# Optimization experiments

Measured on AMD Instinct MI355X. Metric: run time of the kernel, lower is better.

The kernel has to match this reference:

```python
import jax, jax.numpy as jnp
import numpy as np

R, C, H, W = 500, 512, 38, 38      # rois, VGG channels, feature-map HxW (img 608 / 16)
K, HID, POOL, SCALE = 20, 4096, 3, 16
FEAT = C * POOL * POOL             # 4608, matches fc6 in_features


def setup_inputs():
    key = jax.random.key(0)
    ks = jax.random.split(key, 12)
    fmap = jax.random.normal(ks[0], (C, H, W), dtype=jnp.float32)
    # ROIs in original image coords (x1,y1,x2,y2); width/height >= 48 px so that
    # after /16 + floor every ROI is non-degenerate (none filtered out).
    x1 = jax.random.randint(ks[1], (R,), 0, 288)
    y1 = jax.random.randint(ks[2], (R,), 0, 288)
    bw = jax.random.randint(ks[3], (R,), 48, 304)
    bh = jax.random.randint(ks[4], (R,), 48, 304)
    rois = jnp.stack([x1, y1, x1 + bw, y1 + bh], axis=1).astype(jnp.float32)
    label = jax.random.bernoulli(ks[5], 0.3, (K,)).astype(jnp.float32)
    s = 0.01
    W6 = jax.random.normal(ks[6], (FEAT, HID), jnp.float32) * s
    b6 = jnp.zeros((HID,), jnp.float32)
    W7 = jax.random.normal(ks[7], (HID, HID), jnp.float32) * s
    b7 = jnp.zeros((HID,), jnp.float32)
    W8c = jax.random.normal(ks[8], (HID, K), jnp.float32) * s
    b8c = jnp.zeros((K,), jnp.float32)
    W8d = jax.random.normal(ks[9], (HID, K), jnp.float32) * s
    b8d = jnp.zeros((K,), jnp.float32)
    return dict(fmap=fmap, rois=rois, label=label, W6=W6, b6=b6, W7=W7, b7=b7,
                W8c=W8c, b8c=b8c, W8d=W8d, b8d=b8d)


def _roi_pool(fmap, rois):
    # scaled_rois = origin_rois / 16, sliced as integer indices (floor)
    sc = jnp.floor(rois / SCALE).astype(jnp.int32)          # [R,4]
    x1, y1, x2, y2 = sc[:, 0], sc[:, 1], sc[:, 2], sc[:, 3]

    def binmask(lo, hi, size):
        # adaptive-max-pool bins: [lo + floor(j*L/3), lo + ceil((j+1)*L/3))
        L = hi - lo                                          # [R]
        j = jnp.arange(POOL)
        start = lo[:, None] + (j[None, :] * L[:, None]) // POOL
        end = lo[:, None] + (-((-(j[None, :] + 1) * L[:, None]) // POOL))
        pos = jnp.arange(size)
        return (pos[None, None, :] >= start[:, :, None]) & (pos[None, None, :] < end[:, :, None])

    cm = binmask(x1, x2, W)                                  # [R,3,W]
    rm = binmask(y1, y2, H)                                  # [R,3,H]
    neg = jnp.finfo(fmap.dtype).min
    # max over x within each x-bin: [R,C,H,3]
    tmp = jnp.max(jnp.where(cm[:, None, None, :, :], fmap[None, :, :, None, :], neg), axis=-1)
    # max over y within each y-bin: [R,C,3,3]
    pooled = jnp.max(jnp.where(rm[:, None, :, :, None], tmp[:, :, None, :, :], neg), axis=3)
    return pooled.reshape(R, FEAT), sc.astype(jnp.float32)


def _spatial_reg(scores, fc7, rois_sc, label):
    # faithful to original: argsort ascending, index 0 taken as the reference box,
    # and bboxes_iou interprets (x1,y1,x2,y2) as (x,y,w,h) — replicated as-is.
    idx = jnp.argsort(scores, axis=0)                        # [R,K]

    def per_class(idx_k, s_k, lab_k):
        h, rest = idx_k[0], idx_k[1:]
        hb = rois_sc[h]                                      # [4]
        rb = rois_sc[rest]                                   # [R-1,4]
        b1x2, b1y2 = rb[:, 0] + rb[:, 2], rb[:, 1] + rb[:, 3]
        b2x2, b2y2 = hb[0] + hb[2], hb[1] + hb[3]
        iw = jnp.clip(jnp.minimum(b1x2, b2x2) - jnp.maximum(rb[:, 0], hb[0]) + 1, 0)
        ih = jnp.clip(jnp.minimum(b1y2, b2y2) - jnp.maximum(rb[:, 1], hb[1]) + 1, 0)
        inter = iw * ih
        a1 = (b1x2 - rb[:, 0] + 1) * (b1y2 - rb[:, 1] + 1)
        a2 = (b2x2 - hb[0] + 1) * (b2y2 - hb[1] + 1)
        iou = inter / (a1 + a2 - inter)
        m = (iou > 0.6).astype(fc7.dtype)                    # [R-1]
        rf = fc7[rest] * m[:, None]
        diff = (rf - fc7[h]) * s_k[rest][:, None]
        return lab_k * 0.5 * jnp.sum(diff * diff)

    regs = jax.vmap(per_class)(idx.T, scores.T, label)       # [K]
    return jnp.sum(regs) / K


def reference(fmap, rois, label, W6, b6, W7, b7, W8c, b8c, W8d, b8d):
    feat, rois_sc = _roi_pool(fmap, rois)                    # [R,4608]
    fc6 = feat @ W6 + b6
    fc7 = fc6 @ W7 + b7
    pc = jax.nn.softmax(fc7 @ W8c + b8c, axis=1)             # per-roi over classes
    pd = jax.nn.softmax(fc7 @ W8d + b8d, axis=0)             # per-class over rois
    scores = pc * pd                                         # [R,K]
    out = jnp.sum(scores, axis=0)                            # [K], in (0,1)
    bce = -jnp.mean(label * jnp.log(out) + (1.0 - label) * jnp.log(1.0 - out))
    reg = _spatial_reg(scores, fc7, rois_sc, label)
    return scores, bce + reg, reg
```

## Files before the change

kernel.cpp:

```cpp
#include <hip/hip_runtime.h>
#include <cstdint>
#include <cstddef>

#define DEV __device__ __forceinline__

typedef __bf16 bf16_t;
typedef __bf16 bf16x8 __attribute__((ext_vector_type(8)));
typedef float  f32x4  __attribute__((ext_vector_type(4)));
typedef float  f32x2  __attribute__((ext_vector_type(2)));
typedef unsigned int u32x4 __attribute__((ext_vector_type(4)));

DEV bf16_t f2bf(float x) { return (bf16_t)x; }

constexpr int R_ = 500, C_ = 512, H_ = 38, W_ = 38, K_ = 20;
constexpr int HID = 4096, FEAT = 4608, MP = 512;
constexpr int HW = H_ * W_;

constexpr size_t alup(size_t x) { return (x + 255) & ~(size_t)255; }
constexpr size_t O_FMT  = 0;
constexpr size_t O_RSC  = alup(O_FMT  + (size_t)HW*C_*4);
constexpr size_t O_FEAT = alup(O_RSC  + (size_t)R_*4*4);
constexpr size_t O_FC6  = alup(O_FEAT + (size_t)MP*FEAT*2);
constexpr size_t O_FC7  = alup(O_FC6  + (size_t)MP*HID*2);
constexpr size_t O_PC   = alup(O_FC7  + (size_t)MP*HID*4);
constexpr size_t O_LD   = alup(O_PC   + (size_t)R_*K_*4);
constexpr size_t O_AN   = alup(O_LD   + (size_t)R_*K_*4);
constexpr size_t O_OS   = alup(O_AN   + (size_t)MP*4);
constexpr size_t O_HI   = alup(O_OS   + (size_t)K_*4);
constexpr size_t O_D    = alup(O_HI   + (size_t)K_*4);
constexpr size_t O_W8T  = alup(O_D    + (size_t)R_*K_*4);
constexpr size_t O_PART = alup(O_W8T  + (size_t)2*K_*HID*4);
constexpr size_t O_HP   = O_PART;
constexpr size_t O_DP   = O_PART + (size_t)4*1024*1024;

__global__ void __launch_bounds__(256) k_transpose(const float* __restrict__ fmap,
                                                   float* __restrict__ fmapt) {
    __shared__ float tile[32][33];
    int p0 = blockIdx.x * 32, c0 = blockIdx.y * 32;
    int tx = threadIdx.x & 31, ty = threadIdx.x >> 5;
#pragma unroll
    for (int i = 0; i < 4; ++i) {
        int c = c0 + ty + i*8, p = p0 + tx;
        tile[ty + i*8][tx] = (p < HW) ? fmap[(size_t)c*HW + p] : 0.f;
    }
    __syncthreads();
#pragma unroll
    for (int i = 0; i < 4; ++i) {
        int p = p0 + ty + i*8, c = c0 + tx;
        if (p < HW) fmapt[(size_t)p*C_ + c] = tile[tx][ty + i*8];
    }
}

__global__ void __launch_bounds__(256) k_w8t(const float* __restrict__ W8c,
                                             const float* __restrict__ W8d,
                                             float* __restrict__ W8T) {
    int k = blockIdx.x;
    const float* src = (k < K_) ? W8c : W8d;
    int kk = (k < K_) ? k : k - K_;
    for (int i = threadIdx.x; i < HID; i += 256)
        W8T[(size_t)k*HID + i] = src[(size_t)i*K_ + kk];
}

__global__ void __launch_bounds__(256) k_roipool(const float* __restrict__ fmapt,
                                                 const float* __restrict__ rois,
                                                 bf16_t* __restrict__ feat,
                                                 float* __restrict__ rois_sc) {
    int r = blockIdx.x, bin = blockIdx.y, t = threadIdx.x;
    if (r >= R_) {
        feat[(size_t)r*FEAT + (size_t)t*9       + bin] = (bf16_t)0.f;
        feat[(size_t)r*FEAT + (size_t)(t+256)*9 + bin] = (bf16_t)0.f;
        return;
    }
    int x1 = (int)floorf(rois[r*4+0] * 0.0625f);
    int y1 = (int)floorf(rois[r*4+1] * 0.0625f);
    int x2 = (int)floorf(rois[r*4+2] * 0.0625f);
    int y2 = (int)floorf(rois[r*4+3] * 0.0625f);
    if (bin == 0 && t == 0) {
        rois_sc[r*4+0] = (float)x1; rois_sc[r*4+1] = (float)y1;
        rois_sc[r*4+2] = (float)x2; rois_sc[r*4+3] = (float)y2;
    }
    int Lx = x2 - x1, Ly = y2 - y1;
    int pr = bin / 3, px = bin - pr*3;
    int rs = y1 + (pr*Ly)/3, re = y1 + ((pr+1)*Ly + 2)/3;
    int cs = x1 + (px*Lx)/3, ce = x1 + ((px+1)*Lx + 2)/3;
    float m0 = -3.402823466e38f, m1 = -3.402823466e38f;
    for (int y = rs; y < re; ++y) {
        const float* rowp = fmapt + (size_t)(y*W_)*C_;
        for (int x = cs; x < ce; ++x) {
            const float* p = rowp + (size_t)x*C_;
            m0 = fmaxf(m0, p[t]);
            m1 = fmaxf(m1, p[t + 256]);
        }
    }
    feat[(size_t)r*FEAT + (size_t)t*9       + bin] = f2bf(m0);
    feat[(size_t)r*FEAT + (size_t)(t+256)*9 + bin] = f2bf(m1);
}

__global__ void __launch_bounds__(256, 3)
k_gemm(const bf16_t* __restrict__ A, const float* __restrict__ B,
       float* __restrict__ part, int KDIM, int nts) {
    __shared__ bf16_t Asm[2][128*64];
    __shared__ bf16_t Bsm[2][64*64];
    const int t = threadIdx.x;
    const int lane = t & 63, wid = t >> 6;
    const int wr = wid >> 1, wc = wid & 1;

    const int flat = blockIdx.x + 64*blockIdx.y + 256*blockIdx.z;
    const int v = (flat & 7) * 128 + (flat >> 3);
    const int by = v & 3, bx = (v >> 2) & 63, bz = v >> 8;

    const int brow = by * 128, bcol = bx * 64;
    const int kt0 = bz * nts;

    f32x4 acc[4][2] = {};
    f32x2 br[8];
    const int n2 = t & 31, kgl = t >> 5;

    auto stage_A = [&](int kt, int buf) {
        const bf16_t* Ag = A + (size_t)brow*KDIM + kt*64;
#pragma unroll
        for (int i = 0; i < 4; ++i) {
            int s = t + i*256;
            int row = s >> 3;
            int kb = (s & 7) ^ ((row >> 1) & 7);
            const bf16_t* src = Ag + (size_t)row*KDIM + kb*8;
            bf16_t* dst = &Asm[buf][(size_t)(i*256 + (t & ~63)) * 8];
            __builtin_amdgcn_global_load_lds(
                (const __attribute__((address_space(1))) void*)src,
                (__attribute__((address_space(3))) void*)dst, 16, 0, 0);
        }
    };
    auto load_B = [&](int kt) {
        const float* src = B + (size_t)(kt*64 + kgl*8)*HID + bcol + 2*n2;
#pragma unroll
        for (int j = 0; j < 8; ++j)
            br[j] = *reinterpret_cast<const f32x2*>(src + (size_t)j*HID);
    };
    auto write_B = [&](int buf) {
        const int sw = n2 & 7;
        bf16x8 v0, v1;
#pragma unroll
        for (int j = 0; j < 8; ++j) { v0[j] = f2bf(br[j].x); v1[j] = f2bf(br[j].y); }
        *reinterpret_cast<u32x4*>(&Bsm[buf][(size_t)((2*n2    )*8 + (kgl ^ sw)) * 8]) = *reinterpret_cast<u32x4*>(&v0);
        *reinterpret_cast<u32x4*>(&Bsm[buf][(size_t)((2*n2 + 1)*8 + (kgl ^ sw)) * 8]) = *reinterpret_cast<u32x4*>(&v1);
    };

    stage_A(kt0, 0);
    load_B(kt0);
    write_B(0);
    __syncthreads();

    for (int it = 0; it < nts; ++it) {
        const int cur = it & 1;
        if (it + 1 < nts) { stage_A(kt0 + it + 1, cur ^ 1); load_B(kt0 + it + 1); }
#pragma unroll
        for (int kk = 0; kk < 2; ++kk) {
            const int kb = kk*4 + (lane >> 4);
            bf16x8 af[4], bfr[2];
#pragma unroll
            for (int m = 0; m < 4; ++m) {
                int row = wr*64 + m*16 + (lane & 15);
                af[m] = *reinterpret_cast<const bf16x8*>(
                    &Asm[cur][(size_t)(row*8 + (kb ^ ((row >> 1) & 7))) * 8]);
            }
#pragma unroll
            for (int n = 0; n < 2; ++n) {
                int nn = wc*32 + n*16 + (lane & 15);
                bfr[n] = *reinterpret_cast<const bf16x8*>(
                    &Bsm[cur][(size_t)(nn*8 + (kb ^ ((nn >> 1) & 7))) * 8]);
            }
#pragma unroll
            for (int m = 0; m < 4; ++m)
#pragma unroll
                for (int n = 0; n < 2; ++n)
                    acc[m][n] = __builtin_amdgcn_mfma_f32_16x16x32_bf16(af[m], bfr[n], acc[m][n], 0, 0, 0);
        }
        if (it + 1 < nts) { write_B(cur ^ 1); __syncthreads(); }
    }

    float* dst = part + (size_t)bz * MP * HID;
#pragma unroll
    for (int m = 0; m < 4; ++m) {
        int row0 = brow + wr*64 + m*16 + ((lane >> 4) << 2);
#pragma unroll
        for (int n = 0; n < 2; ++n) {
            int col = bcol + wc*32 + n*16 + (lane & 15);
#pragma unroll
            for (int j = 0; j < 4; ++j)
                dst[(size_t)(row0 + j)*HID + col] = acc[m][n][j];
        }
    }
}

__global__ void __launch_bounds__(256) k_reduce(const float* __restrict__ part,
                                                const float* __restrict__ bias,
                                                bf16_t* __restrict__ ob, float* __restrict__ of,
                                                int ksplit) {
    size_t idx = ((size_t)blockIdx.x*256 + threadIdx.x) * 4;
    f32x4 s = *reinterpret_cast<const f32x4*>(part + idx);
    for (int ss = 1; ss < ksplit; ++ss)
        s += *reinterpret_cast<const f32x4*>(part + (size_t)ss*MP*HID + idx);
    int col = (int)(idx & (HID - 1));
    s += *reinterpret_cast<const f32x4*>(bias + col);
    if (ob) {
#pragma unroll
        for (int j = 0; j < 4; ++j) ob[idx + j] = f2bf(s[j]);
    } else {
        *reinterpret_cast<f32x4*>(of + idx) = s;
    }
}

template<int NOUT, bool SELF>
__global__ void __launch_bounds__(256) k_dotcols(const float* __restrict__ fc7,
        const float* __restrict__ Bmat, const int* __restrict__ bidx,
        float* __restrict__ partial) {
    constexpr int NO = NOUT + (SELF ? 1 : 0);
    constexpr int SLICE = NOUT*16 + 4;
    __shared__ float Bs[8 * SLICE];
    const int rb = blockIdx.x, kb = blockIdx.y, t = threadIdx.x;
    const int k0 = kb * 128;
    for (int i = t; i < NOUT*32; i += 256) {
        int o = i >> 5, c = i & 31;
        const float* src = bidx ? fc7 + (size_t)bidx[o]*HID : Bmat + (size_t)o*HID;
        f32x4 v = *reinterpret_cast<const f32x4*>(src + k0 + c*4);
        *reinterpret_cast<f32x4*>(&Bs[(c >> 2)*SLICE + o*16 + (c & 3)*4]) = v;
    }
    __syncthreads();
    const int lane = t & 63, w = t >> 6;
    const int ri = lane >> 3, kk = lane & 7;
    const int r0 = rb*64 + w*16 + ri*2;
    f32x4 x0[4], x1[4];
    const float* f0 = fc7 + (size_t)r0*HID + k0 + kk*16;
#pragma unroll
    for (int j = 0; j < 4; ++j) {
        x0[j] = *reinterpret_cast<const f32x4*>(f0 + j*4);
        x1[j] = *reinterpret_cast<const f32x4*>(f0 + HID + j*4);
    }
    float acc0[NO], acc1[NO];
#pragma unroll
    for (int o = 0; o < NOUT; ++o) {
        f32x4 s0 = {}, s1 = {};
#pragma unroll
        for (int j = 0; j < 4; ++j) {
            f32x4 wv = *reinterpret_cast<const f32x4*>(&Bs[kk*SLICE + o*16 + j*4]);
            s0 += x0[j] * wv;
            s1 += x1[j] * wv;
        }
        acc0[o] = s0[0]+s0[1]+s0[2]+s0[3];
        acc1[o] = s1[0]+s1[1]+s1[2]+s1[3];
    }
    if (SELF) {
        f32x4 s0 = {}, s1 = {};
#pragma unroll
        for (int j = 0; j < 4; ++j) { s0 += x0[j]*x0[j]; s1 += x1[j]*x1[j]; }
        acc0[NO-1] = s0[0]+s0[1]+s0[2]+s0[3];
        acc1[NO-1] = s1[0]+s1[1]+s1[2]+s1[3];
    }
#pragma unroll
    for (int o = 0; o < NO; ++o) {
#pragma unroll
        for (int m = 1; m < 8; m <<= 1) {
            acc0[o] += __shfl_xor(acc0[o], m, 64);
            acc1[o] += __shfl_xor(acc1[o], m, 64);
        }
    }
    if (kk == 0) {
#pragma unroll
        for (int o = 0; o < NO; ++o) {
            partial[((size_t)kb*MP + r0    )*NO + o] = acc0[o];
            partial[((size_t)kb*MP + r0 + 1)*NO + o] = acc1[o];
        }
    }
}

__global__ void __launch_bounds__(64) k_headred(const float* __restrict__ hpart,
        const float* __restrict__ b8c, const float* __restrict__ b8d,
        float* __restrict__ pc, float* __restrict__ ld, float* __restrict__ An) {
    int r = blockIdx.x, t = threadIdx.x;
    __shared__ float lcs[20];
    if (t < 41) {
        float s = 0.f;
        for (int kb = 0; kb < 32; ++kb) s += hpart[((size_t)kb*MP + r)*41 + t];
        if (t < 20)      lcs[t] = s + b8c[t];
        else if (t < 40) ld[r*K_ + (t-20)] = s + b8d[t-20];
        else             An[r] = s;
    }
    __syncthreads();
    if (t == 0) {
        float mx = lcs[0];
#pragma unroll
        for (int k = 1; k < 20; ++k) mx = fmaxf(mx, lcs[k]);
        float sum = 0.f, e[20];
#pragma unroll
        for (int k = 0; k < 20; ++k) { e[k] = expf(lcs[k] - mx); sum += e[k]; }
        float inv = 1.f / sum;
#pragma unroll
        for (int k = 0; k < 20; ++k) pc[r*K_ + k] = e[k] * inv;
    }
}

__global__ void __launch_bounds__(64) k_dmatred(const float* __restrict__ dpart,
                                                float* __restrict__ D) {
    int r = blockIdx.x, t = threadIdx.x;
    if (t < 20) {
        float s = 0.f;
        for (int kb = 0; kb < 32; ++kb) s += dpart[((size_t)kb*MP + r)*20 + t];
        D[r*K_ + t] = s;
    }
}

__global__ void __launch_bounds__(256) k_pd(const float* __restrict__ ld,
        const float* __restrict__ pc, float* __restrict__ scores,
        float* __restrict__ out_sum, int* __restrict__ h_idx) {
    int k = blockIdx.x, t = threadIdx.x;
    __shared__ float sh[4];
    float m = -3.402823466e38f;
    for (int r = t; r < R_; r += 256) m = fmaxf(m, ld[r*K_ + k]);
    for (int off = 1; off < 64; off <<= 1) m = fmaxf(m, __shfl_xor(m, off, 64));
    if ((t & 63) == 0) sh[t >> 6] = m;
    __syncthreads();
    m = fmaxf(fmaxf(sh[0], sh[1]), fmaxf(sh[2], sh[3]));
    __syncthreads();
    float s = 0.f;
    for (int r = t; r < R_; r += 256) s += expf(ld[r*K_ + k] - m);
    for (int off = 1; off < 64; off <<= 1) s += __shfl_xor(s, off, 64);
    if ((t & 63) == 0) sh[t >> 6] = s;
    __syncthreads();
    s = sh[0] + sh[1] + sh[2] + sh[3];
    float inv = 1.f / s;

    float osum = 0.f, bv = 3.402823466e38f; int bi = 0x7fffffff;
    for (int r = t; r < R_; r += 256) {
        float p  = expf(ld[r*K_ + k] - m) * inv;
        float sc = pc[r*K_ + k] * p;
        scores[r*K_ + k] = sc;
        osum += sc;
        if (sc < bv || (sc == bv && r < bi)) { bv = sc; bi = r; }
    }
    for (int off = 1; off < 64; off <<= 1) osum += __shfl_xor(osum, off, 64);
    for (int off = 1; off < 64; off <<= 1) {
        float v2 = __shfl_xor(bv, off, 64);
        int   i2 = __shfl_xor(bi, off, 64);
        if (v2 < bv || (v2 == bv && i2 < bi)) { bv = v2; bi = i2; }
    }
    __shared__ float so[4], mv[4]; __shared__ int mi[4];
    if ((t & 63) == 0) { so[t >> 6] = osum; mv[t >> 6] = bv; mi[t >> 6] = bi; }
    __syncthreads();
    if (t == 0) {
        out_sum[k] = so[0] + so[1] + so[2] + so[3];
        float v = mv[0]; int i = mi[0];
        for (int w = 1; w < 4; ++w)
            if (mv[w] < v || (mv[w] == v && mi[w] < i)) { v = mv[w]; i = mi[w]; }
        h_idx[k] = i;
    }
}

__global__ void __launch_bounds__(256) k_final(const float* __restrict__ out_sum,
        const int* __restrict__ h_idx, const float* __restrict__ label,
        const float* __restrict__ scores, const float* __restrict__ D,
        const float* __restrict__ An, const float* __restrict__ rois_sc,
        float* __restrict__ dout) {
    int t = threadIdx.x;
    __shared__ float bsh[20];
    if (t < 20) {
        float o = out_sum[t], lab = label[t];
        bsh[t] = lab * logf(o) + (1.f - lab) * logf(1.f - o);
    }
    __syncthreads();

    float rp = 0.f;
    for (int i = t; i < R_*K_; i += 256) {
        int r = i / 20, k = i - r*20;
        int h = h_idx[k];
        if (r == h) continue;
        float lab = label[k];
        if (lab == 0.f) continue;
        float s = scores[r*K_ + k];
        const float* rb = rois_sc + r*4;
        const float* hb = rois_sc + h*4;
        float b1x2 = rb[0] + rb[2], b1y2 = rb[1] + rb[3];
        float b2x2 = hb[0] + hb[2], b2y2 = hb[1] + hb[3];
        float iw = fmaxf(fminf(b1x2, b2x2) - fmaxf(rb[0], hb[0]) + 1.f, 0.f);
        float ih = fmaxf(fminf(b1y2, b2y2) - fmaxf(rb[1], hb[1]) + 1.f, 0.f);
        float inter = iw * ih;
        float a1 = (b1x2 - rb[0] + 1.f) * (b1y2 - rb[1] + 1.f);
        float a2 = (b2x2 - hb[0] + 1.f) * (b2y2 - hb[1] + 1.f);
        float iou = inter / (a1 + a2 - inter);
        float mm = (iou > 0.6f) ? 1.f : 0.f;
        float term = mm * (An[r] - 2.f * D[r*K_ + k]) + An[h];
        rp += lab * 0.5f * s * s * term;
    }
    for (int off = 1; off < 64; off <<= 1) rp += __shfl_xor(rp, off, 64);
    __shared__ float rsh[4];
    if ((t & 63) == 0) rsh[t >> 6] = rp;
    __syncthreads();
    if (t == 0) {
        float reg = (rsh[0] + rsh[1] + rsh[2] + rsh[3]) / (float)K_;
        float b = 0.f;
        for (int k = 0; k < 20; ++k) b += bsh[k];
        float bce = -b / (float)K_;
        dout[R_*K_]     = bce + reg;
        dout[R_*K_ + 1] = reg;
    }
}

extern "C" void kernel_launch(void* const* d_in, const int* in_sizes, int n_in,
                              void* d_out, int out_size, void* d_ws, size_t ws_size,
                              hipStream_t stream) {
    const float* fmap  = (const float*)d_in[0];
    const float* rois  = (const float*)d_in[1];
    const float* label = (const float*)d_in[2];
    const float* W6    = (const float*)d_in[3];
    const float* b6    = (const float*)d_in[4];
    const float* W7    = (const float*)d_in[5];
    const float* b7    = (const float*)d_in[6];
    const float* W8c   = (const float*)d_in[7];
    const float* b8c   = (const float*)d_in[8];
    const float* W8d   = (const float*)d_in[9];
    const float* b8d   = (const float*)d_in[10];
    char* ws = (char*)d_ws;
    float* out = (float*)d_out;

    float*  fmapt = (float*)(ws + O_FMT);
    float*  roisc = (float*)(ws + O_RSC);
    bf16_t* feat  = (bf16_t*)(ws + O_FEAT);
    bf16_t* fc6   = (bf16_t*)(ws + O_FC6);
    float*  fc7   = (float*)(ws + O_FC7);
    float*  pc    = (float*)(ws + O_PC);
    float*  ld    = (float*)(ws + O_LD);
    float*  An    = (float*)(ws + O_AN);
    float*  osum  = (float*)(ws + O_OS);
    int*    hidx  = (int*)(ws + O_HI);
    float*  Dm    = (float*)(ws + O_D);
    float*  w8t   = (float*)(ws + O_W8T);
    float*  part  = (float*)(ws + O_PART);
    float*  hpart = (float*)(ws + O_HP);
    float*  dpart = (float*)(ws + O_DP);

    const int ksplit = 4;

    k_transpose<<<dim3((HW + 31)/32, C_/32), dim3(256), 0, stream>>>(fmap, fmapt);
    k_w8t      <<<dim3(2*K_),   dim3(256), 0, stream>>>(W8c, W8d, w8t);
    k_roipool  <<<dim3(MP, 9),  dim3(256), 0, stream>>>(fmapt, rois, feat, roisc);

    k_gemm  <<<dim3(HID/64, MP/128, ksplit), dim3(256), 0, stream>>>(feat, W6, part, FEAT, (FEAT/64)/ksplit);
    k_reduce<<<dim3((MP*HID)/1024), dim3(256), 0, stream>>>(part, b6, fc6, (float*)nullptr, ksplit);

    k_gemm  <<<dim3(HID/64, MP/128, ksplit), dim3(256), 0, stream>>>(fc6, W7, part, HID, (HID/64)/ksplit);
    k_reduce<<<dim3((MP*HID)/1024), dim3(256), 0, stream>>>(part, b7, (bf16_t*)nullptr, fc7, ksplit);

    k_dotcols<40, true><<<dim3(MP/64, HID/128), dim3(256), 0, stream>>>(fc7, w8t, (const int*)nullptr, hpart);
    k_headred<<<dim3(R_), dim3(64), 0, stream>>>(hpart, b8c, b8d, pc, ld, An);
    k_pd     <<<dim3(K_), dim3(256), 0, stream>>>(ld, pc, out, osum, hidx);
    k_dotcols<20, false><<<dim3(MP/64, HID/128), dim3(256), 0, stream>>>(fc7, (const float*)nullptr, hidx, dpart);
    k_dmatred<<<dim3(R_), dim3(64), 0, stream>>>(dpart, Dm);
    k_final  <<<dim3(1),  dim3(256), 0, stream>>>(osum, hidx, label, out, Dm, An, roisc, out);
}
```

Before: 199.1 us.

## Widen GEMM tile to 128x128 and deepen A/B prefetch pipeline

The fc6/fc7 GEMM moves from 128x64 to 128x128 output tiles, so each wave computes a 4x4 set of MFMA accumulators and each B load is reused across more rows. The A tile now uses triple-buffered async global-to-LDS loads and B uses two register sets, so loads run two k-steps ahead. Barriers become explicit s_waitcnt plus s_barrier calls. This halves the grid to 512 blocks and raises register and LDS use, which lowers the occupancy target from 3 to 2 blocks per CU. The main loop assumes an even tile count per split.

```diff
diff --git a/kernel.cpp b/kernel.cpp
--- a/kernel.cpp
+++ b/kernel.cpp
@@ -96,27 +96,27 @@
     feat[(size_t)r*FEAT + (size_t)(t+256)*9 + bin] = f2bf(m1);
 }
 
-__global__ void __launch_bounds__(256, 3)
+__global__ void __launch_bounds__(256, 2)
 k_gemm(const bf16_t* __restrict__ A, const float* __restrict__ B,
        float* __restrict__ part, int KDIM, int nts) {
-    __shared__ bf16_t Asm[2][128*64];
-    __shared__ bf16_t Bsm[2][64*64];
+    __shared__ bf16_t Asm[3][128*64];
+    __shared__ bf16_t Bsm[2][128*64];
     const int t = threadIdx.x;
     const int lane = t & 63, wid = t >> 6;
     const int wr = wid >> 1, wc = wid & 1;
 
-    const int flat = blockIdx.x + 64*blockIdx.y + 256*blockIdx.z;
-    const int v = (flat & 7) * 128 + (flat >> 3);
-    const int by = v & 3, bx = (v >> 2) & 63, bz = v >> 8;
-
-    const int brow = by * 128, bcol = bx * 64;
+    const int flat = blockIdx.x + 32*blockIdx.y + 128*blockIdx.z;
+    const int q = 16 * gridDim.z;
+    const int v = (flat & 7) * q + (flat >> 3);
+    const int by = v & 3, bx = (v >> 2) & 31, bz = v >> 7;
+
+    const int brow = by * 128, bcol = bx * 128;
     const int kt0 = bz * nts;
 
-    f32x4 acc[4][2] = {};
-    f32x2 br[8];
-    const int n2 = t & 31, kgl = t >> 5;
-
-    auto stage_A = [&](int kt, int buf) {
+    f32x4 acc[4][4] = {};
+    const int n2 = t & 63, kgl = t >> 6;
+
+    auto stage_A = [&](int kt, bf16_t* dstbuf) {
         const bf16_t* Ag = A + (size_t)brow*KDIM + kt*64;
 #pragma unroll
         for (int i = 0; i < 4; ++i) {
@@ -124,58 +124,81 @@
             int row = s >> 3;
             int kb = (s & 7) ^ ((row >> 1) & 7);
             const bf16_t* src = Ag + (size_t)row*KDIM + kb*8;
-            bf16_t* dst = &Asm[buf][(size_t)(i*256 + (t & ~63)) * 8];
+            bf16_t* dst = dstbuf + (size_t)(i*256 + (t & ~63)) * 8;
             __builtin_amdgcn_global_load_lds(
                 (const __attribute__((address_space(1))) void*)src,
                 (__attribute__((address_space(3))) void*)dst, 16, 0, 0);
         }
     };
-    auto load_B = [&](int kt) {
-        const float* src = B + (size_t)(kt*64 + kgl*8)*HID + bcol + 2*n2;
-#pragma unroll
-        for (int j = 0; j < 8; ++j)
+    auto load_B = [&](int kt, f32x2* br) {
+        const float* src = B + (size_t)(kt*64 + kgl*16)*HID + bcol + 2*n2;
+#pragma unroll
+        for (int j = 0; j < 16; ++j)
             br[j] = *reinterpret_cast<const f32x2*>(src + (size_t)j*HID);
     };
-    auto write_B = [&](int buf) {
+    auto write_B = [&](f32x2* br, bf16_t* buf) {
         const int sw = n2 & 7;
         bf16x8 v0, v1;
 #pragma unroll
-        for (int j = 0; j < 8; ++j) { v0[j] = f2bf(br[j].x); v1[j] = f2bf(br[j].y); }
-        *reinterpret_cast<u32x4*>(&Bsm[buf][(size_t)((2*n2    )*8 + (kgl ^ sw)) * 8]) = *reinterpret_cast<u32x4*>(&v0);
-        *reinterpret_cast<u32x4*>(&Bsm[buf][(size_t)((2*n2 + 1)*8 + (kgl ^ sw)) * 8]) = *reinterpret_cast<u32x4*>(&v1);
+        for (int j = 0; j < 8; ++j) { v0[j] = f2bf(br[j].x); v1[j] = f2bf(br[j+8].x); }
+        *reinterpret_cast<u32x4*>(&buf[(size_t)((2*n2)*8 + ((kgl*2    ) ^ sw)) * 8]) = *reinterpret_cast<u32x4*>(&v0);
+        *reinterpret_cast<u32x4*>(&buf[(size_t)((2*n2)*8 + ((kgl*2 + 1) ^ sw)) * 8]) = *reinterpret_cast<u32x4*>(&v1);
+#pragma unroll
+        for (int j = 0; j < 8; ++j) { v0[j] = f2bf(br[j].y); v1[j] = f2bf(br[j+8].y); }
+        *reinterpret_cast<u32x4*>(&buf[(size_t)((2*n2+1)*8 + ((kgl*2    ) ^ sw)) * 8]) = *reinterpret_cast<u32x4*>(&v0);
+        *reinterpret_cast<u32x4*>(&buf[(size_t)((2*n2+1)*8 + ((kgl*2 + 1) ^ sw)) * 8]) = *reinterpret_cast<u32x4*>(&v1);
     };
 
-    stage_A(kt0, 0);
-    load_B(kt0);
-    write_B(0);
-    __syncthreads();
-
-    for (int it = 0; it < nts; ++it) {
-        const int cur = it & 1;
-        if (it + 1 < nts) { stage_A(kt0 + it + 1, cur ^ 1); load_B(kt0 + it + 1); }
+    bf16_t* pa0 = &Asm[0][0]; bf16_t* pa1 = &Asm[1][0]; bf16_t* pa2 = &Asm[2][0];
+    bf16_t* pb0 = &Bsm[0][0]; bf16_t* pb1 = &Bsm[1][0];
+    f32x2 brA[16], brB[16];
+
+    stage_A(kt0 + 0, pa0);
+    load_B (kt0 + 0, brA);
+    stage_A(kt0 + 1, pa1);
+    load_B (kt0 + 1, brB);
+    write_B(brA, pb0);
+    asm volatile("s_waitcnt lgkmcnt(0)" ::: "memory");
+    __builtin_amdgcn_s_barrier();
+    __builtin_amdgcn_sched_barrier(0);
+
+    auto body = [&](int tt, f32x2* prev, f32x2* next) {
+        if (tt + 2 < nts) { stage_A(kt0 + tt + 2, pa2); load_B(kt0 + tt + 2, next); }
 #pragma unroll
         for (int kk = 0; kk < 2; ++kk) {
             const int kb = kk*4 + (lane >> 4);
-            bf16x8 af[4], bfr[2];
+            bf16x8 af[4], bfr[4];
 #pragma unroll
             for (int m = 0; m < 4; ++m) {
                 int row = wr*64 + m*16 + (lane & 15);
                 af[m] = *reinterpret_cast<const bf16x8*>(
-                    &Asm[cur][(size_t)(row*8 + (kb ^ ((row >> 1) & 7))) * 8]);
+                    pa0 + (size_t)(row*8 + (kb ^ ((row >> 1) & 7))) * 8);
             }
 #pragma unroll
-            for (int n = 0; n < 2; ++n) {
-                int nn = wc*32 + n*16 + (lane & 15);
+            for (int n = 0; n < 4; ++n) {
+                int nn = wc*64 + n*16 + (lane & 15);
                 bfr[n] = *reinterpret_cast<const bf16x8*>(
-                    &Bsm[cur][(size_t)(nn*8 + (kb ^ ((nn >> 1) & 7))) * 8]);
+                    pb0 + (size_t)(nn*8 + (kb ^ ((nn >> 1) & 7))) * 8);
             }
 #pragma unroll
             for (int m = 0; m < 4; ++m)
 #pragma unroll
-                for (int n = 0; n < 2; ++n)
+                for (int n = 0; n < 4; ++n)
                     acc[m][n] = __builtin_amdgcn_mfma_f32_16x16x32_bf16(af[m], bfr[n], acc[m][n], 0, 0, 0);
         }
-        if (it + 1 < nts) { write_B(cur ^ 1); __syncthreads(); }
+        if (tt + 1 < nts) {
+            write_B(prev, pb1);
+            asm volatile("s_waitcnt lgkmcnt(0)" ::: "memory");
+            __builtin_amdgcn_s_barrier();
+            __builtin_amdgcn_sched_barrier(0);
+        }
+        bf16_t* ta = pa0; pa0 = pa1; pa1 = pa2; pa2 = ta;
+        bf16_t* tb = pb0; pb0 = pb1; pb1 = tb;
+    };
+
+    for (int it = 0; it < nts; it += 2) {
+        body(it,     brB, brA);
+        body(it + 1, brA, brB);
     }
 
     float* dst = part + (size_t)bz * MP * HID;
@@ -183,8 +206,8 @@
     for (int m = 0; m < 4; ++m) {
         int row0 = brow + wr*64 + m*16 + ((lane >> 4) << 2);
 #pragma unroll
-        for (int n = 0; n < 2; ++n) {
-            int col = bcol + wc*32 + n*16 + (lane & 15);
+        for (int n = 0; n < 4; ++n) {
+            int col = bcol + wc*64 + n*16 + (lane & 15);
 #pragma unroll
             for (int j = 0; j < 4; ++j)
                 dst[(size_t)(row0 + j)*HID + col] = acc[m][n][j];
@@ -443,10 +466,10 @@
     k_w8t      <<<dim3(2*K_),   dim3(256), 0, stream>>>(W8c, W8d, w8t);
     k_roipool  <<<dim3(MP, 9),  dim3(256), 0, stream>>>(fmapt, rois, feat, roisc);
 
-    k_gemm  <<<dim3(HID/64, MP/128, ksplit), dim3(256), 0, stream>>>(feat, W6, part, FEAT, (FEAT/64)/ksplit);
+    k_gemm  <<<dim3(HID/128, MP/128, ksplit), dim3(256), 0, stream>>>(feat, W6, part, FEAT, (FEAT/64)/ksplit);
     k_reduce<<<dim3((MP*HID)/1024), dim3(256), 0, stream>>>(part, b6, fc6, (float*)nullptr, ksplit);
 
-    k_gemm  <<<dim3(HID/64, MP/128, ksplit), dim3(256), 0, stream>>>(fc6, W7, part, HID, (HID/64)/ksplit);
+    k_gemm  <<<dim3(HID/128, MP/128, ksplit), dim3(256), 0, stream>>>(fc6, W7, part, HID, (HID/64)/ksplit);
     k_reduce<<<dim3((MP*HID)/1024), dim3(256), 0, stream>>>(part, b7, (bf16_t*)nullptr, fc7, ksplit);
 
     k_dotcols<40, true><<<dim3(MP/64, HID/128), dim3(256), 0, stream>>>(fc7, w8t, (const int*)nullptr, hpart);
```

Measured after the change: 177.9 us, median of 2. 10.6% less time.

## Replace split-K partial buffers with atomic accumulation and enlarge GEMM tiles

Applied to the files above, without the earlier changes.

The split-K GEMM now adds its partial results and a scaled bias straight into zeroed fp32 outputs with atomics. This removes the partial-buffer write and the separate reduce kernels, and the dotcols partial reductions get the same treatment. The GEMM tile widens to 128x128 with split-K raised to 8, and the transpose and W8 prep kernels merge into one launch. This costs memsets, atomic contention, a separate bf16 cast kernel, lower occupancy, and a summation order that is no longer deterministic.

```diff
diff --git a/kernel.cpp b/kernel.cpp
--- a/kernel.cpp
+++ b/kernel.cpp
@@ -15,50 +15,53 @@
 constexpr int R_ = 500, C_ = 512, H_ = 38, W_ = 38, K_ = 20;
 constexpr int HID = 4096, FEAT = 4608, MP = 512;
 constexpr int HW = H_ * W_;
+constexpr int KSPLIT = 8;
 
 constexpr size_t alup(size_t x) { return (x + 255) & ~(size_t)255; }
 constexpr size_t O_FMT  = 0;
 constexpr size_t O_RSC  = alup(O_FMT  + (size_t)HW*C_*4);
 constexpr size_t O_FEAT = alup(O_RSC  + (size_t)R_*4*4);
 constexpr size_t O_FC6  = alup(O_FEAT + (size_t)MP*FEAT*2);
-constexpr size_t O_FC7  = alup(O_FC6  + (size_t)MP*HID*2);
+constexpr size_t O_FC6F = alup(O_FC6  + (size_t)MP*HID*2);
+constexpr size_t O_FC7  = alup(O_FC6F + (size_t)MP*HID*4);
 constexpr size_t O_PC   = alup(O_FC7  + (size_t)MP*HID*4);
 constexpr size_t O_LD   = alup(O_PC   + (size_t)R_*K_*4);
 constexpr size_t O_AN   = alup(O_LD   + (size_t)R_*K_*4);
 constexpr size_t O_OS   = alup(O_AN   + (size_t)MP*4);
 constexpr size_t O_HI   = alup(O_OS   + (size_t)K_*4);
-constexpr size_t O_D    = alup(O_HI   + (size_t)K_*4);
-constexpr size_t O_W8T  = alup(O_D    + (size_t)R_*K_*4);
-constexpr size_t O_PART = alup(O_W8T  + (size_t)2*K_*HID*4);
-constexpr size_t O_HP   = O_PART;
-constexpr size_t O_DP   = O_PART + (size_t)4*1024*1024;
-
-__global__ void __launch_bounds__(256) k_transpose(const float* __restrict__ fmap,
-                                                   float* __restrict__ fmapt) {
-    __shared__ float tile[32][33];
-    int p0 = blockIdx.x * 32, c0 = blockIdx.y * 32;
-    int tx = threadIdx.x & 31, ty = threadIdx.x >> 5;
-#pragma unroll
-    for (int i = 0; i < 4; ++i) {
-        int c = c0 + ty + i*8, p = p0 + tx;
-        tile[ty + i*8][tx] = (p < HW) ? fmap[(size_t)c*HW + p] : 0.f;
-    }
-    __syncthreads();
-#pragma unroll
-    for (int i = 0; i < 4; ++i) {
-        int p = p0 + ty + i*8, c = c0 + tx;
-        if (p < HW) fmapt[(size_t)p*C_ + c] = tile[tx][ty + i*8];
-    }
-}
-
-__global__ void __launch_bounds__(256) k_w8t(const float* __restrict__ W8c,
-                                             const float* __restrict__ W8d,
-                                             float* __restrict__ W8T) {
-    int k = blockIdx.x;
-    const float* src = (k < K_) ? W8c : W8d;
-    int kk = (k < K_) ? k : k - K_;
-    for (int i = threadIdx.x; i < HID; i += 256)
-        W8T[(size_t)k*HID + i] = src[(size_t)i*K_ + kk];
+constexpr size_t O_W8T  = alup(O_HI   + (size_t)K_*4);
+constexpr size_t O_HL   = alup(O_W8T  + (size_t)2*K_*HID*4);
+constexpr size_t O_D    = alup(O_HL   + (size_t)MP*41*4);
+constexpr size_t O_END  = alup(O_D    + (size_t)MP*K_*4);
+
+__global__ void __launch_bounds__(256) k_prep(const float* __restrict__ fmap,
+                                              float* __restrict__ fmapt,
+                                              const float* __restrict__ W8c,
+                                              const float* __restrict__ W8d,
+                                              float* __restrict__ W8T) {
+    int b = blockIdx.x;
+    if (b < 736) {
+        __shared__ float tile[32][33];
+        int p0 = (b % 46) * 32, c0 = (b / 46) * 32;
+        int tx = threadIdx.x & 31, ty = threadIdx.x >> 5;
+#pragma unroll
+        for (int i = 0; i < 4; ++i) {
+            int c = c0 + ty + i*8, p = p0 + tx;
+            tile[ty + i*8][tx] = (p < HW) ? fmap[(size_t)c*HW + p] : 0.f;
+        }
+        __syncthreads();
+#pragma unroll
+        for (int i = 0; i < 4; ++i) {
+            int p = p0 + ty + i*8, c = c0 + tx;
+            if (p < HW) fmapt[(size_t)p*C_ + c] = tile[tx][ty + i*8];
+        }
+    } else {
+        int k = b - 736;
+        const float* src = (k < K_) ? W8c : W8d;
+        int kk = (k < K_) ? k : k - K_;
+        for (int i = threadIdx.x; i < HID; i += 256)
+            W8T[(size_t)k*HID + i] = src[(size_t)i*K_ + kk];
+    }
 }
 
 __global__ void __launch_bounds__(256) k_roipool(const float* __restrict__ fmapt,
@@ -96,25 +99,26 @@
     feat[(size_t)r*FEAT + (size_t)(t+256)*9 + bin] = f2bf(m1);
 }
 
-__global__ void __launch_bounds__(256, 3)
+__global__ void __launch_bounds__(256, 2)
 k_gemm(const bf16_t* __restrict__ A, const float* __restrict__ B,
-       float* __restrict__ part, int KDIM, int nts) {
+       float* __restrict__ outF32, const float* __restrict__ bias, float bscale,
+       int KDIM, int nts) {
     __shared__ bf16_t Asm[2][128*64];
-    __shared__ bf16_t Bsm[2][64*64];
+    __shared__ bf16_t Bsm[2][128*64];
     const int t = threadIdx.x;
     const int lane = t & 63, wid = t >> 6;
     const int wr = wid >> 1, wc = wid & 1;
 
-    const int flat = blockIdx.x + 64*blockIdx.y + 256*blockIdx.z;
+    const int flat = blockIdx.x + 32*blockIdx.y + 128*blockIdx.z;
     const int v = (flat & 7) * 128 + (flat >> 3);
-    const int by = v & 3, bx = (v >> 2) & 63, bz = v >> 8;
-
-    const int brow = by * 128, bcol = bx * 64;
+    const int by = v & 3, bz = (v >> 2) & 7, bx = v >> 5;
+
+    const int brow = by * 128, bcol = bx * 128;
     const int kt0 = bz * nts;
 
-    f32x4 acc[4][2] = {};
-    f32x2 br[8];
-    const int n2 = t & 31, kgl = t >> 5;
+    f32x4 acc[4][4] = {};
+    f32x2 br[16];
+    const int n2 = t & 63, kgl = t >> 6;
 
     auto stage_A = [&](int kt, int buf) {
         const bf16_t* Ag = A + (size_t)brow*KDIM + kt*64;
@@ -131,18 +135,22 @@
         }
     };
     auto load_B = [&](int kt) {
-        const float* src = B + (size_t)(kt*64 + kgl*8)*HID + bcol + 2*n2;
-#pragma unroll
-        for (int j = 0; j < 8; ++j)
+        const float* src = B + (size_t)(kt*64 + kgl*16)*HID + bcol + 2*n2;
+#pragma unroll
+        for (int j = 0; j < 16; ++j)
             br[j] = *reinterpret_cast<const f32x2*>(src + (size_t)j*HID);
     };
     auto write_B = [&](int buf) {
         const int sw = n2 & 7;
         bf16x8 v0, v1;
 #pragma unroll
-        for (int j = 0; j < 8; ++j) { v0[j] = f2bf(br[j].x); v1[j] = f2bf(br[j].y); }
-        *reinterpret_cast<u32x4*>(&Bsm[buf][(size_t)((2*n2    )*8 + (kgl ^ sw)) * 8]) = *reinterpret_cast<u32x4*>(&v0);
-        *reinterpret_cast<u32x4*>(&Bsm[buf][(size_t)((2*n2 + 1)*8 + (kgl ^ sw)) * 8]) = *reinterpret_cast<u32x4*>(&v1);
+        for (int j = 0; j < 8; ++j) { v0[j] = f2bf(br[j].x); v1[j] = f2bf(br[j+8].x); }
+        *reinterpret_cast<u32x4*>(&Bsm[buf][(size_t)((2*n2)*8 + ((kgl*2    ) ^ sw)) * 8]) = *reinterpret_cast<u32x4*>(&v0);
+        *reinterpret_cast<u32x4*>(&Bsm[buf][(size_t)((2*n2)*8 + ((kgl*2 + 1) ^ sw)) * 8]) = *reinterpret_cast<u32x4*>(&v1);
+#pragma unroll
+        for (int j = 0; j < 8; ++j) { v0[j] = f2bf(br[j].y); v1[j] = f2bf(br[j+8].y); }
+        *reinterpret_cast<u32x4*>(&Bsm[buf][(size_t)((2*n2+1)*8 + ((kgl*2    ) ^ sw)) * 8]) = *reinterpret_cast<u32x4*>(&v0);
+        *reinterpret_cast<u32x4*>(&Bsm[buf][(size_t)((2*n2+1)*8 + ((kgl*2 + 1) ^ sw)) * 8]) = *reinterpret_cast<u32x4*>(&v1);
     };
 
     stage_A(kt0, 0);
@@ -156,7 +164,7 @@
 #pragma unroll
         for (int kk = 0; kk < 2; ++kk) {
             const int kb = kk*4 + (lane >> 4);
-            bf16x8 af[4], bfr[2];
+            bf16x8 af[4], bfr[4];
 #pragma unroll
             for (int m = 0; m < 4; ++m) {
                 int row = wr*64 + m*16 + (lane & 15);
@@ -164,56 +172,49 @@
                     &Asm[cur][(size_t)(row*8 + (kb ^ ((row >> 1) & 7))) * 8]);
             }
 #pragma unroll
-            for (int n = 0; n < 2; ++n) {
-                int nn = wc*32 + n*16 + (lane & 15);
+            for (int n = 0; n < 4; ++n) {
+                int nn = wc*64 + n*16 + (lane & 15);
                 bfr[n] = *reinterpret_cast<const bf16x8*>(
                     &Bsm[cur][(size_t)(nn*8 + (kb ^ ((nn >> 1) & 7))) * 8]);
             }
 #pragma unroll
             for (int m = 0; m < 4; ++m)
 #pragma unroll
-                for (int n = 0; n < 2; ++n)
+                for (int n = 0; n < 4; ++n)
                     acc[m][n] = __builtin_amdgcn_mfma_f32_16x16x32_bf16(af[m], bfr[n], acc[m][n], 0, 0, 0);
         }
         if (it + 1 < nts) { write_B(cur ^ 1); __syncthreads(); }
     }
 
-    float* dst = part + (size_t)bz * MP * HID;
 #pragma unroll
     for (int m = 0; m < 4; ++m) {
         int row0 = brow + wr*64 + m*16 + ((lane >> 4) << 2);
 #pragma unroll
-        for (int n = 0; n < 2; ++n) {
-            int col = bcol + wc*32 + n*16 + (lane & 15);
+        for (int n = 0; n < 4; ++n) {
+            int col = bcol + wc*64 + n*16 + (lane & 15);
+            float bv = bias[col] * bscale;
 #pragma unroll
             for (int j = 0; j < 4; ++j)
-                dst[(size_t)(row0 + j)*HID + col] = acc[m][n][j];
-        }
-    }
-}
-
-__global__ void __launch_bounds__(256) k_reduce(const float* __restrict__ part,
-                                                const float* __restrict__ bias,
-                                                bf16_t* __restrict__ ob, float* __restrict__ of,
-                                                int ksplit) {
-    size_t idx = ((size_t)blockIdx.x*256 + threadIdx.x) * 4;
-    f32x4 s = *reinterpret_cast<const f32x4*>(part + idx);
-    for (int ss = 1; ss < ksplit; ++ss)
-        s += *reinterpret_cast<const f32x4*>(part + (size_t)ss*MP*HID + idx);
-    int col = (int)(idx & (HID - 1));
-    s += *reinterpret_cast<const f32x4*>(bias + col);
-    if (ob) {
-#pragma unroll
-        for (int j = 0; j < 4; ++j) ob[idx + j] = f2bf(s[j]);
-    } else {
-        *reinterpret_cast<f32x4*>(of + idx) = s;
-    }
+                unsafeAtomicAdd(&outF32[(size_t)(row0 + j)*HID + col], acc[m][n][j] + bv);
+        }
+    }
+}
+
+__global__ void __launch_bounds__(256) k_cast(const float* __restrict__ in,
+                                              bf16_t* __restrict__ out) {
+    size_t idx = ((size_t)blockIdx.x*256 + threadIdx.x) * 8;
+    f32x4 a = *reinterpret_cast<const f32x4*>(in + idx);
+    f32x4 b = *reinterpret_cast<const f32x4*>(in + idx + 4);
+    bf16x8 v;
+#pragma unroll
+    for (int j = 0; j < 4; ++j) { v[j] = f2bf(a[j]); v[4+j] = f2bf(b[j]); }
+    *reinterpret_cast<bf16x8*>(out + idx) = v;
 }
 
 template<int NOUT, bool SELF>
 __global__ void __launch_bounds__(256) k_dotcols(const float* __restrict__ fc7,
         const float* __restrict__ Bmat, const int* __restrict__ bidx,
-        float* __restrict__ partial) {
+        float* __restrict__ outacc) {
     constexpr int NO = NOUT + (SELF ? 1 : 0);
     constexpr int SLICE = NOUT*16 + 4;
     __shared__ float Bs[8 * SLICE];
@@ -267,20 +268,19 @@
     if (kk == 0) {
 #pragma unroll
         for (int o = 0; o < NO; ++o) {
-            partial[((size_t)kb*MP + r0    )*NO + o] = acc0[o];
-            partial[((size_t)kb*MP + r0 + 1)*NO + o] = acc1[o];
-        }
-    }
-}
-
-__global__ void __launch_bounds__(64) k_headred(const float* __restrict__ hpart,
+            unsafeAtomicAdd(&outacc[(size_t)r0*NO + o],       acc0[o]);
+            unsafeAtomicAdd(&outacc[(size_t)(r0 + 1)*NO + o], acc1[o]);
+        }
+    }
+}
+
+__global__ void __launch_bounds__(64) k_headred(const float* __restrict__ hl,
         const float* __restrict__ b8c, const float* __restrict__ b8d,
         float* __restrict__ pc, float* __restrict__ ld, float* __restrict__ An) {
     int r = blockIdx.x, t = threadIdx.x;
     __shared__ float lcs[20];
     if (t < 41) {
-        float s = 0.f;
-        for (int kb = 0; kb < 32; ++kb) s += hpart[((size_t)kb*MP + r)*41 + t];
+        float s = hl[(size_t)r*41 + t];
         if (t < 20)      lcs[t] = s + b8c[t];
         else if (t < 40) ld[r*K_ + (t-20)] = s + b8d[t-20];
         else             An[r] = s;
@@ -296,16 +296,6 @@
         float inv = 1.f / sum;
 #pragma unroll
         for (int k = 0; k < 20; ++k) pc[r*K_ + k] = e[k] * inv;
-    }
-}
-
-__global__ void __launch_bounds__(64) k_dmatred(const float* __restrict__ dpart,
-                                                float* __restrict__ D) {
-    int r = blockIdx.x, t = threadIdx.x;
-    if (t < 20) {
-        float s = 0.f;
-        for (int kb = 0; kb < 32; ++kb) s += dpart[((size_t)kb*MP + r)*20 + t];
-        D[r*K_ + t] = s;
     }
 }
 
@@ -425,34 +415,33 @@
     float*  roisc = (float*)(ws + O_RSC);
     bf16_t* feat  = (bf16_t*)(ws + O_FEAT);
     bf16_t* fc6   = (bf16_t*)(ws + O_FC6);
+    float*  fc6f  = (float*)(ws + O_FC6F);
     float*  fc7   = (float*)(ws + O_FC7);
     float*  pc    = (float*)(ws + O_PC);
     float*  ld    = (float*)(ws + O_LD);
     float*  An    = (float*)(ws + O_AN);
     float*  osum  = (float*)(ws + O_OS);
     int*    hidx  = (int*)(ws + O_HI);
+    float*  w8t   = (float*)(ws + O_W8T);
+    float*  hl    = (float*)(ws + O_HL);
     float*  Dm    = (float*)(ws + O_D);
-    float*  w8t   = (float*)(ws + O_W8T);
-    float*  part  = (float*)(ws + O_PART);
-    float*  hpart = (float*)(ws + O_HP);
-    float*  dpart = (float*)(ws + O_DP);
-
-    const int ksplit = 4;
-
-    k_transpose<<<dim3((HW + 31)/32, C_/32), dim3(256), 0, stream>>>(fmap, fmapt);
-    k_w8t      <<<dim3(2*K_),   dim3(256), 0, stream>>>(W8c, W8d, w8t);
-    k_roipool  <<<dim3(MP, 9),  dim3(256), 0, stream>>>(fmapt, rois, feat, roisc);
-
-    k_gemm  <<<dim3(HID/64, MP/128, ksplit), dim3(256), 0, stream>>>(feat, W6, part, FEAT, (FEAT/64)/ksplit);
-    k_reduce<<<dim3((MP*HID)/1024), dim3(256), 0, stream>>>(part, b6, fc6, (float*)nullptr, ksplit);
-
-    k_gemm  <<<dim3(HID/64, MP/128, ksplit), dim3(256), 0, stream>>>(fc6, W7, part, HID, (HID/64)/ksplit);
-    k_reduce<<<dim3((MP*HID)/1024), dim3(256), 0, stream>>>(part, b7, (bf16_t*)nullptr, fc7, ksplit);
-
-    k_dotcols<40, true><<<dim3(MP/64, HID/128), dim3(256), 0, stream>>>(fc7, w8t, (const int*)nullptr, hpart);
-    k_headred<<<dim3(R_), dim3(64), 0, stream>>>(hpart, b8c, b8d, pc, ld, An);
+
+    hipMemsetAsync(fc6f, 0, (size_t)MP*HID*4, stream);
+    hipMemsetAsync(fc7,  0, (size_t)MP*HID*4, stream);
+    hipMemsetAsync(hl,   0, O_END - O_HL, stream);
+
+    k_prep   <<<dim3(736 + 2*K_), dim3(256), 0, stream>>>(fmap, fmapt, W8c, W8d, w8t);
+    k_roipool<<<dim3(MP, 9),      dim3(256), 0, stream>>>(fmapt, rois, feat, roisc);
+
+    k_gemm<<<dim3(HID/128, MP/128, KSPLIT), dim3(256), 0, stream>>>(
+        feat, W6, fc6f, b6, 1.f/KSPLIT, FEAT, (FEAT/64)/KSPLIT);
+    k_cast<<<dim3((MP*HID)/2048), dim3(256), 0, stream>>>(fc6f, fc6);
+    k_gemm<<<dim3(HID/128, MP/128, KSPLIT), dim3(256), 0, stream>>>(
+        fc6, W7, fc7, b7, 1.f/KSPLIT, HID, (HID/64)/KSPLIT);
+
+    k_dotcols<40, true><<<dim3(MP/64, HID/128), dim3(256), 0, stream>>>(fc7, w8t, (const int*)nullptr, hl);
+    k_headred<<<dim3(R_), dim3(64), 0, stream>>>(hl, b8c, b8d, pc, ld, An);
     k_pd     <<<dim3(K_), dim3(256), 0, stream>>>(ld, pc, out, osum, hidx);
-    k_dotcols<20, false><<<dim3(MP/64, HID/128), dim3(256), 0, stream>>>(fc7, (const float*)nullptr, hidx, dpart);
-    k_dmatred<<<dim3(R_), dim3(64), 0, stream>>>(dpart, Dm);
+    k_dotcols<20, false><<<dim3(MP/64, HID/128), dim3(256), 0, stream>>>(fc7, (const float*)nullptr, hidx, Dm);
     k_final  <<<dim3(1),  dim3(256), 0, stream>>>(osum, hidx, label, out, Dm, An, roisc, out);
 }
```

After: 355.0 us. 78.3% more time.
